# Optimization experiments

Hardware: AMD Instinct MI355X
Metric: run time of the kernel (lower is better)

The kernel has to match this reference:

```python
import jax, jax.numpy as jnp
import numpy as np

B, C, H, W = 4, 256, 32, 32
NUM_HEADS = 8
DK = C // NUM_HEADS


def _conv1x1(x_bcn, Wt, b):
    # x_bcn: [B, C, N]; Wt: [C_out, C_in]; b: [C_out]
    return jnp.einsum('oc,bcn->bon', Wt, x_bcn) + b[None, :, None]


def setup_inputs() -> dict:
    key = jax.random.key(0)
    ks = jax.random.split(key, 12)
    shp = (B, C, H, W)
    s = 1.0 / np.sqrt(C)
    return {
        'x0': jax.random.normal(ks[0], shp, jnp.float32),
        'x1': jax.random.normal(ks[1], shp, jnp.float32),
        'x2': jax.random.normal(ks[2], shp, jnp.float32),
        'gamma': jnp.ones((1,), jnp.float32),
        'gamma_1': jnp.ones((1,), jnp.float32),
        'gamma_2': jnp.ones((1,), jnp.float32),
        'Wq': jax.random.normal(ks[3], (C, C), jnp.float32) * s,
        'bq': jnp.zeros((C,), jnp.float32),
        'Wk': jax.random.normal(ks[4], (C, C), jnp.float32) * s,
        'bk': jnp.zeros((C,), jnp.float32),
        'Wv': jax.random.normal(ks[5], (C, C), jnp.float32) * s,
        'bv': jnp.zeros((C,), jnp.float32),
        'Wo': jax.random.normal(ks[6], (C, C), jnp.float32) * s,
        'bo': jnp.zeros((C,), jnp.float32),
    }


def reference(x0, x1, x2, gamma, gamma_1, gamma_2, Wq, bq, Wk, bk, Wv, bv, Wo, bo):
    h, dk = NUM_HEADS, DK
    N = H * W
    s0 = gamma * x0
    s1 = gamma_1 * x1
    s2 = gamma_2 * x2
    s0f = s0.reshape(B, C, N)
    streams = jnp.stack([s0f, s1.reshape(B, C, N), s2.reshape(B, C, N)], axis=1)  # [B,3,C,N]
    # Q: [B, h, N, dk]
    Q = _conv1x1(s0f, Wq, bq).reshape(B, h, dk, N).transpose(0, 1, 3, 2)
    kv_in = streams.reshape(B * 3, C, N)
    # K, V: [B, 3, h, dk, N] -> [B, h, 3N, dk]
    K = _conv1x1(kv_in, Wk, bk).reshape(B, 3, h, dk, N).transpose(0, 2, 1, 4, 3).reshape(B, h, 3 * N, dk)
    V = _conv1x1(kv_in, Wv, bv).reshape(B, 3, h, dk, N).transpose(0, 2, 1, 4, 3).reshape(B, h, 3 * N, dk)
    scores = jnp.einsum('bhqd,bhkd->bhqk', Q, K) / jnp.sqrt(jnp.float32(dk))  # [B,h,N,3N]
    attn = jax.nn.softmax(scores, axis=-1)
    out = jnp.einsum('bhqk,bhkd->bhqd', attn, V)  # [B,h,N,dk]
    out = out.transpose(0, 1, 3, 2).reshape(B, C, N)  # [B,C,N]
    fused = _conv1x1(out, Wo, bo).reshape(B, C, H, W)
    return fused
```

## Files before the change

kernel.cpp:

```cpp
#include <hip/hip_runtime.h>

typedef short bf16x8 __attribute__((ext_vector_type(8)));
typedef float f32x4  __attribute__((ext_vector_type(4)));
typedef short sh4    __attribute__((ext_vector_type(4)));
typedef float fl4    __attribute__((ext_vector_type(4)));
typedef unsigned u32x2 __attribute__((ext_vector_type(2)));
typedef unsigned u32x4 __attribute__((ext_vector_type(4)));

#define B_N  4
#define C_N  256
#define NH_N 8
#define DK_N 32
#define N_N  1024
#define KN_N 3072

#if defined(__has_builtin)
#if __has_builtin(__builtin_amdgcn_permlane32_swap) && __has_builtin(__builtin_amdgcn_permlane16_swap)
#define USE_PERMLANE 1
#endif
#endif
#ifndef USE_PERMLANE
#define USE_PERMLANE 0
#endif

__device__ __forceinline__ short f2bf(float f) {
    union { float f; unsigned u; } v; v.f = f;
    unsigned r = v.u + 0x7fffu + ((v.u >> 16) & 1u);
    return (short)(r >> 16);
}
__device__ __forceinline__ unsigned fbits(float f) {
    union { float f; unsigned u; } v; v.f = f; return v.u;
}

__device__ __forceinline__ int stg_idx(int c, int n) {
    return c * 64 + ((((n >> 2) ^ (c >> 2)) & 15) << 2) + (n & 3);
}

__global__ __launch_bounds__(256) void prep_kernel(
    const float* __restrict__ x0, const float* __restrict__ x1,
    const float* __restrict__ x2, const float* __restrict__ g0,
    const float* __restrict__ g1, const float* __restrict__ g2,
    const float* __restrict__ Wq, const float* __restrict__ Wk,
    const float* __restrict__ Wv, const float* __restrict__ Wo,
    short* __restrict__ Xt, short* __restrict__ Wbf) {
    __shared__ float stage[4096];
    int bx = blockIdx.x, t = threadIdx.x;
    if (bx >= 192) {
        int e = (bx - 192) * 4096 + t * 16;
        int m = e >> 16, off = e & 65535;
        const float* src = (m == 0) ? Wq : (m == 1) ? Wk : (m == 2) ? Wv : Wo;
        short* dst = Wbf + m * 65536 + off;
#pragma unroll
        for (int j = 0; j < 4; ++j) {
            fl4 v = *reinterpret_cast<const fl4*>(src + off + j * 4);
            sh4 o;
            o.x = f2bf(v.x); o.y = f2bf(v.y); o.z = f2bf(v.z); o.w = f2bf(v.w);
            *reinterpret_cast<sh4*>(dst + j * 4) = o;
        }
        return;
    }
    int bs = bx >> 4;
    int n0 = (bx & 15) << 6;
    int b = bs / 3, s = bs - b * 3;
    const float* xs = (s == 0) ? x0 : (s == 1) ? x1 : x2;
    float g = (s == 0) ? g0[0] : (s == 1) ? g1[0] : g2[0];
    const float* srcb = xs + (size_t)b * C_N * N_N;
    int n4 = (t & 15) << 2;
    for (int ch = 0; ch < 4; ++ch) {
        int c0 = ch << 6;
#pragma unroll
        for (int r = 0; r < 4; ++r) {
            int cl = (t >> 4) + (r << 4);
            fl4 v = *reinterpret_cast<const fl4*>(srcb + (size_t)(c0 + cl) * N_N + n0 + n4);
            v.x *= g; v.y *= g; v.z *= g; v.w *= g;
            *reinterpret_cast<fl4*>(&stage[stg_idx(cl, n4)]) = v;
        }
        __syncthreads();
#pragma unroll
        for (int j = 0; j < 2; ++j) {
            int u = t + (j << 8);
            int nl = u >> 3, cg = (u & 7) << 3;
            union { bf16x8 v8; short s16[8]; } pk;
#pragma unroll
            for (int i = 0; i < 8; ++i) pk.s16[i] = f2bf(stage[stg_idx(cg + i, nl)]);
            size_t rowsh = ((size_t)bs * N_N + n0 + nl) * C_N;
            unsigned cb = ((unsigned)((c0 + cg) * 2)) ^ ((unsigned)((nl & 7) << 4));
            *reinterpret_cast<bf16x8*>((char*)Xt + rowsh * 2 + cb) = pk.v8;
        }
        __syncthreads();
    }
}

__global__ __launch_bounds__(256) void qkv_kernel(
    const short* __restrict__ Wbf, const float* __restrict__ bq,
    const float* __restrict__ bk, const float* __restrict__ bv,
    const short* __restrict__ Xt,
    short* __restrict__ Qs, short* __restrict__ Ks, short* __restrict__ Vt) {
    __shared__ short Bt[16384];
    int b = blockIdx.z, mt = blockIdx.y, ct = blockIdx.x;
    int s = ct >> 4, n0 = (ct & 15) << 6;
    int t = threadIdx.x, lane = t & 63, w = t >> 6;
    int l16 = lane & 15, quad = lane >> 4;
    int m0 = mt << 6;
    bool hasQ = (s == 0);

    const char* gsrc = (const char*)(Xt + (((size_t)(b * 3 + s)) * N_N + n0) * C_N);
    char* ldst = (char*)Bt;
#pragma unroll
    for (int i = 0; i < 8; ++i) {
        int off = ((w << 3) + i) << 10;
        __builtin_amdgcn_global_load_lds(
            (const __attribute__((address_space(1))) void*)(gsrc + off + lane * 16),
            (__attribute__((address_space(3))) void*)(ldst + off), 16, 0, 0);
    }
    __syncthreads();

    f32x4 aq[4], ak[4], av[4];
#pragma unroll
    for (int i = 0; i < 4; ++i) {
        aq[i] = f32x4{0.f, 0.f, 0.f, 0.f};
        ak[i] = f32x4{0.f, 0.f, 0.f, 0.f};
        av[i] = f32x4{0.f, 0.f, 0.f, 0.f};
    }
    const short* WqA = Wbf;
    const short* WkA = Wbf + 65536;
    const short* WvA = Wbf + 131072;
    int arow = m0 + (w << 4) + l16;
    unsigned xv = (unsigned)((l16 & 7) << 4);
    const char* btb = (const char*)Bt;
#pragma unroll
    for (int kc = 0; kc < 256; kc += 32) {
        unsigned colb = ((unsigned)((kc + quad * 8) * 2)) ^ xv;
        bf16x8 bt0 = *reinterpret_cast<const bf16x8*>(btb + ((0  + l16) << 9) + colb);
        bf16x8 bt1 = *reinterpret_cast<const bf16x8*>(btb + ((16 + l16) << 9) + colb);
        bf16x8 bt2 = *reinterpret_cast<const bf16x8*>(btb + ((32 + l16) << 9) + colb);
        bf16x8 bt3 = *reinterpret_cast<const bf16x8*>(btb + ((48 + l16) << 9) + colb);
        bf16x8 wk = *reinterpret_cast<const bf16x8*>(WkA + (size_t)arow * C_N + kc + quad * 8);
        ak[0] = __builtin_amdgcn_mfma_f32_16x16x32_bf16(wk, bt0, ak[0], 0, 0, 0);
        ak[1] = __builtin_amdgcn_mfma_f32_16x16x32_bf16(wk, bt1, ak[1], 0, 0, 0);
        ak[2] = __builtin_amdgcn_mfma_f32_16x16x32_bf16(wk, bt2, ak[2], 0, 0, 0);
        ak[3] = __builtin_amdgcn_mfma_f32_16x16x32_bf16(wk, bt3, ak[3], 0, 0, 0);
        bf16x8 wv = *reinterpret_cast<const bf16x8*>(WvA + (size_t)arow * C_N + kc + quad * 8);
        av[0] = __builtin_amdgcn_mfma_f32_16x16x32_bf16(wv, bt0, av[0], 0, 0, 0);
        av[1] = __builtin_amdgcn_mfma_f32_16x16x32_bf16(wv, bt1, av[1], 0, 0, 0);
        av[2] = __builtin_amdgcn_mfma_f32_16x16x32_bf16(wv, bt2, av[2], 0, 0, 0);
        av[3] = __builtin_amdgcn_mfma_f32_16x16x32_bf16(wv, bt3, av[3], 0, 0, 0);
        if (hasQ) {
            bf16x8 wq = *reinterpret_cast<const bf16x8*>(WqA + (size_t)arow * C_N + kc + quad * 8);
            aq[0] = __builtin_amdgcn_mfma_f32_16x16x32_bf16(wq, bt0, aq[0], 0, 0, 0);
            aq[1] = __builtin_amdgcn_mfma_f32_16x16x32_bf16(wq, bt1, aq[1], 0, 0, 0);
            aq[2] = __builtin_amdgcn_mfma_f32_16x16x32_bf16(wq, bt2, aq[2], 0, 0, 0);
            aq[3] = __builtin_amdgcn_mfma_f32_16x16x32_bf16(wq, bt3, aq[3], 0, 0, 0);
        }
    }
    __syncthreads();

    short* SMq = Bt;
    short* SMk = Bt + 5120;
    short* SMv = Bt + 10240;
    int row0 = m0 + (w << 4) + (quad << 2);
    int dk0 = ((w & 1) << 4) + (quad << 2);
    {
        float kb0 = bk[row0], kb1 = bk[row0 + 1], kb2 = bk[row0 + 2], kb3 = bk[row0 + 3];
        short* Tp = SMk + (w >> 1) * 2560 + dk0;
#pragma unroll
        for (int nt = 0; nt < 4; ++nt) {
            int pos = (nt << 4) + l16;
            sh4 pk;
            pk.x = f2bf(ak[nt][0] + kb0); pk.y = f2bf(ak[nt][1] + kb1);
            pk.z = f2bf(ak[nt][2] + kb2); pk.w = f2bf(ak[nt][3] + kb3);
            *reinterpret_cast<sh4*>(Tp + pos * 40) = pk;
        }
    }
    if (hasQ) {
        const float QSCALE = 0.17677669529663687f * 1.4426950408889634f;
        float qb0 = bq[row0], qb1 = bq[row0 + 1], qb2 = bq[row0 + 2], qb3 = bq[row0 + 3];
        short* Tp = SMq + (w >> 1) * 2560 + dk0;
#pragma unroll
        for (int nt = 0; nt < 4; ++nt) {
            int pos = (nt << 4) + l16;
            sh4 pk;
            pk.x = f2bf((aq[nt][0] + qb0) * QSCALE); pk.y = f2bf((aq[nt][1] + qb1) * QSCALE);
            pk.z = f2bf((aq[nt][2] + qb2) * QSCALE); pk.w = f2bf((aq[nt][3] + qb3) * QSCALE);
            *reinterpret_cast<sh4*>(Tp + pos * 40) = pk;
        }
    }
    {
        int crow = (w << 4) + (quad << 2);
        float vb0 = bv[m0 + crow], vb1 = bv[m0 + crow + 1];
        float vb2 = bv[m0 + crow + 2], vb3 = bv[m0 + crow + 3];
#pragma unroll
        for (int nt = 0; nt < 4; ++nt) {
            int pos = (nt << 4) + l16;
            SMv[(crow + 0) * 72 + pos] = f2bf(av[nt][0] + vb0);
            SMv[(crow + 1) * 72 + pos] = f2bf(av[nt][1] + vb1);
            SMv[(crow + 2) * 72 + pos] = f2bf(av[nt][2] + vb2);
            SMv[(crow + 3) * 72 + pos] = f2bf(av[nt][3] + vb3);
        }
    }
    __syncthreads();

    {
        int pos_l = t >> 2, seg = t & 3;
#pragma unroll
        for (int hl = 0; hl < 2; ++hl) {
            int h = 2 * mt + hl;
            bf16x8 kv = *reinterpret_cast<const bf16x8*>(SMk + hl * 2560 + pos_l * 40 + seg * 8);
            *reinterpret_cast<bf16x8*>(
                Ks + ((size_t)(b * NH_N + h) * KN_N + s * N_N + n0) * DK_N + t * 8) = kv;
            if (hasQ) {
                bf16x8 qv = *reinterpret_cast<const bf16x8*>(SMq + hl * 2560 + pos_l * 40 + seg * 8);
                *reinterpret_cast<bf16x8*>(
                    Qs + ((size_t)(b * NH_N + h) * N_N + n0) * DK_N + t * 8) = qv;
            }
        }
#pragma unroll
        for (int i = 0; i < 2; ++i) {
            int chn = t + (i << 8);
            int row = chn >> 3, seg2 = chn & 7;
            bf16x8 vv = *reinterpret_cast<const bf16x8*>(SMv + row * 72 + seg2 * 8);
            int co = m0 + row;
            int h = co >> 5, d = co & 31;
            *reinterpret_cast<bf16x8*>(
                Vt + ((size_t)(b * NH_N + h) * DK_N + d) * KN_N + s * N_N + n0 + seg2 * 8) = vv;
        }
    }
}

struct Frags { bf16x8 k0, k1, k2, k3, v00, v01, v10, v11; };

__device__ __forceinline__ Frags ldfr(const short* Kp, const short* Vp0, int k0) {
    Frags f;
    f.k0  = *reinterpret_cast<const bf16x8*>(Kp + (k0 +  0) * DK_N);
    f.k1  = *reinterpret_cast<const bf16x8*>(Kp + (k0 + 16) * DK_N);
    f.k2  = *reinterpret_cast<const bf16x8*>(Kp + (k0 + 32) * DK_N);
    f.k3  = *reinterpret_cast<const bf16x8*>(Kp + (k0 + 48) * DK_N);
    f.v00 = *reinterpret_cast<const bf16x8*>(Vp0 + k0);
    f.v01 = *reinterpret_cast<const bf16x8*>(Vp0 + 16 * KN_N + k0);
    f.v10 = *reinterpret_cast<const bf16x8*>(Vp0 + k0 + 32);
    f.v11 = *reinterpret_cast<const bf16x8*>(Vp0 + 16 * KN_N + k0 + 32);
    return f;
}

#define EXPPACK(sv, Ra, Rb, LACC) {                             \
    float p0 = __builtin_amdgcn_exp2f(sv[0]);                   \
    float p1 = __builtin_amdgcn_exp2f(sv[1]);                   \
    float p2 = __builtin_amdgcn_exp2f(sv[2]);                   \
    float p3 = __builtin_amdgcn_exp2f(sv[3]);                   \
    LACC += (p0 + p1) + (p2 + p3);                              \
    Ra = __builtin_amdgcn_perm(fbits(p1), fbits(p0), 0x07060302u); \
    Rb = __builtin_amdgcn_perm(fbits(p3), fbits(p2), 0x07060302u); \
}

#if USE_PERMLANE
#define PVSTEP(RA0, RA1, RB0, RB1, VF0, VF1, O0, O1) {                 \
    unsigned x0 = RA0, y0 = RB0, x1 = RA1, y1 = RB1;                   \
    u32x2 r_;                                                          \
    r_ = __builtin_amdgcn_permlane32_swap(x0, y0, false, false); x0 = r_.x; y0 = r_.y; \
    r_ = __builtin_amdgcn_permlane16_swap(x0, y0, false, false); x0 = r_.x; y0 = r_.y; \
    r_ = __builtin_amdgcn_permlane32_swap(x1, y1, false, false); x1 = r_.x; y1 = r_.y; \
    r_ = __builtin_amdgcn_permlane16_swap(x1, y1, false, false); x1 = r_.x; y1 = r_.y; \
    union { u32x4 u; bf16x8 b; } pf_; pf_.u = u32x4{x0, x1, y0, y1};   \
    __builtin_amdgcn_s_setprio(1);                                     \
    O0 = __builtin_amdgcn_mfma_f32_16x16x32_bf16(VF0, pf_.b, O0, 0, 0, 0); \
    O1 = __builtin_amdgcn_mfma_f32_16x16x32_bf16(VF1, pf_.b, O1, 0, 0, 0); \
    __builtin_amdgcn_s_setprio(0);                                     \
}
#else
#define PVSTEP(RA0, RA1, RB0, RB1, VF0, VF1, O0, O1) {                 \
    union { u32x2 u; sh4 s; } wa_, wb_;                                \
    wa_.u = u32x2{RA0, RA1}; wb_.u = u32x2{RB0, RB1};                  \
    *reinterpret_cast<sh4*>(&PT[w][l16][quad * 4])      = wa_.s;       \
    *reinterpret_cast<sh4*>(&PT[w][l16][16 + quad * 4]) = wb_.s;       \
    bf16x8 pf_ = *reinterpret_cast<bf16x8*>(&PT[w][l16][quad * 8]);    \
    O0 = __builtin_amdgcn_mfma_f32_16x16x32_bf16(VF0, pf_, O0, 0, 0, 0); \
    O1 = __builtin_amdgcn_mfma_f32_16x16x32_bf16(VF1, pf_, O1, 0, 0, 0); \
}
#endif

#define PROCJ(f, QF, LACC, O0, O1) {                                     \
    __builtin_amdgcn_s_setprio(1);                                       \
    f32x4 s0 = __builtin_amdgcn_mfma_f32_16x16x32_bf16(f.k0, QF, zero, 0, 0, 0); \
    f32x4 s1 = __builtin_amdgcn_mfma_f32_16x16x32_bf16(f.k1, QF, zero, 0, 0, 0); \
    f32x4 s2 = __builtin_amdgcn_mfma_f32_16x16x32_bf16(f.k2, QF, zero, 0, 0, 0); \
    f32x4 s3 = __builtin_amdgcn_mfma_f32_16x16x32_bf16(f.k3, QF, zero, 0, 0, 0); \
    __builtin_amdgcn_s_setprio(0);                                       \
    unsigned R00, R01, R10, R11, R20, R21, R30, R31;                     \
    EXPPACK(s0, R00, R01, LACC); EXPPACK(s1, R10, R11, LACC);            \
    EXPPACK(s2, R20, R21, LACC); EXPPACK(s3, R30, R31, LACC);            \
    PVSTEP(R00, R01, R10, R11, f.v00, f.v01, O0, O1);                    \
    PVSTEP(R20, R21, R30, R31, f.v10, f.v11, O0, O1);                    \
}

#define PROCALL(f) {                                                     \
    PROCJ(f, qf0, la0, o00, o01);                                        \
    PROCJ(f, qf1, la1, o10, o11);                                        \
    PROCJ(f, qf2, la2, o20, o21);                                        \
    PROCJ(f, qf3, la3, o30, o31);                                        \
}

__global__ __launch_bounds__(256, 2) void attn_kernel(
    const short* __restrict__ Qs, const short* __restrict__ Ks,
    const short* __restrict__ Vt, short* __restrict__ Ot) {
    __shared__ float OL[4][64][36];
    __shared__ float Ll[4][64];
#if !USE_PERMLANE
    __shared__ short PT[4][16][36];
#endif

    int bh = blockIdx.x;
    int q0 = blockIdx.y * 64;
    int t = threadIdx.x, lane = t & 63, w = t >> 6;
    int l16 = lane & 15, quad = lane >> 4;

    const short* Qbase = Qs + ((size_t)bh * N_N + q0 + l16) * DK_N + quad * 8;
    bf16x8 qf0 = *reinterpret_cast<const bf16x8*>(Qbase + 0 * 16 * DK_N);
    bf16x8 qf1 = *reinterpret_cast<const bf16x8*>(Qbase + 1 * 16 * DK_N);
    bf16x8 qf2 = *reinterpret_cast<const bf16x8*>(Qbase + 2 * 16 * DK_N);
    bf16x8 qf3 = *reinterpret_cast<const bf16x8*>(Qbase + 3 * 16 * DK_N);
    const short* Kp  = Ks + ((size_t)bh * KN_N + l16) * DK_N + quad * 8;
    const short* Vp0 = Vt + ((size_t)bh * DK_N + l16) * KN_N + quad * 8;

    const f32x4 zero = {0.f, 0.f, 0.f, 0.f};
    f32x4 o00 = zero, o01 = zero, o10 = zero, o11 = zero;
    f32x4 o20 = zero, o21 = zero, o30 = zero, o31 = zero;
    float la0 = 0.f, la1 = 0.f, la2 = 0.f, la3 = 0.f;
    int kbase = w * 768;

    Frags cur = ldfr(Kp, Vp0, kbase);
#pragma unroll 2
    for (int i = 0; i < 11; ++i) {
        Frags nxt = ldfr(Kp, Vp0, kbase + (i + 1) * 64);
        PROCALL(cur);
        cur = nxt;
    }
    PROCALL(cur);

    la0 += __shfl_xor(la0, 16); la0 += __shfl_xor(la0, 32);
    la1 += __shfl_xor(la1, 16); la1 += __shfl_xor(la1, 32);
    la2 += __shfl_xor(la2, 16); la2 += __shfl_xor(la2, 32);
    la3 += __shfl_xor(la3, 16); la3 += __shfl_xor(la3, 32);

    *reinterpret_cast<fl4*>(&OL[w][ 0 + l16][quad * 4])      = o00;
    *reinterpret_cast<fl4*>(&OL[w][ 0 + l16][16 + quad * 4]) = o01;
    *reinterpret_cast<fl4*>(&OL[w][16 + l16][quad * 4])      = o10;
    *reinterpret_cast<fl4*>(&OL[w][16 + l16][16 + quad * 4]) = o11;
    *reinterpret_cast<fl4*>(&OL[w][32 + l16][quad * 4])      = o20;
    *reinterpret_cast<fl4*>(&OL[w][32 + l16][16 + quad * 4]) = o21;
    *reinterpret_cast<fl4*>(&OL[w][48 + l16][quad * 4])      = o30;
    *reinterpret_cast<fl4*>(&OL[w][48 + l16][16 + quad * 4]) = o31;
    if (quad == 0) {
        Ll[w][ 0 + l16] = la0;
        Ll[w][16 + l16] = la1;
        Ll[w][32 + l16] = la2;
        Ll[w][48 + l16] = la3;
    }
    __syncthreads();

    int q = t >> 2, d0 = (t & 3) * 8;
    float rl = 1.0f / (Ll[0][q] + Ll[1][q] + Ll[2][q] + Ll[3][q]);
    fl4 a0 = *reinterpret_cast<fl4*>(&OL[0][q][d0]);
    fl4 a1 = *reinterpret_cast<fl4*>(&OL[0][q][d0 + 4]);
#pragma unroll
    for (int s = 1; s < 4; ++s) {
        fl4 b0 = *reinterpret_cast<fl4*>(&OL[s][q][d0]);
        fl4 b1 = *reinterpret_cast<fl4*>(&OL[s][q][d0 + 4]);
        a0.x += b0.x; a0.y += b0.y; a0.z += b0.z; a0.w += b0.w;
        a1.x += b1.x; a1.y += b1.y; a1.z += b1.z; a1.w += b1.w;
    }
    union { sh4 s[2]; bf16x8 v; } pk;
    pk.s[0].x = f2bf(a0.x * rl); pk.s[0].y = f2bf(a0.y * rl);
    pk.s[0].z = f2bf(a0.z * rl); pk.s[0].w = f2bf(a0.w * rl);
    pk.s[1].x = f2bf(a1.x * rl); pk.s[1].y = f2bf(a1.y * rl);
    pk.s[1].z = f2bf(a1.z * rl); pk.s[1].w = f2bf(a1.w * rl);
    int b = bh >> 3, h = bh & 7;
    *reinterpret_cast<bf16x8*>(
        Ot + ((size_t)b * N_N + q0 + q) * C_N + h * DK_N + d0) = pk.v;
}

__global__ __launch_bounds__(256) void oproj_kernel(
    const short* __restrict__ Wo_bf, const float* __restrict__ bo,
    const short* __restrict__ Ot, float* __restrict__ out) {
    __shared__ float OS[64][36];
    int b = blockIdx.z, mt = blockIdx.y, ct = blockIdx.x;
    int t = threadIdx.x;
    int lane = t & 63, w = t >> 6;
    int l16 = lane & 15, quad = lane >> 4;
    int m0 = mt * 64, n0 = ct * 32;
    const short* Bsrc = Ot + ((size_t)b * N_N + n0) * C_N;
    int arow = m0 + w * 16 + l16;

    f32x4 acc[2];
    acc[0] = f32x4{0.f, 0.f, 0.f, 0.f};
    acc[1] = f32x4{0.f, 0.f, 0.f, 0.f};

#pragma unroll
    for (int kc = 0; kc < 256; kc += 32) {
        bf16x8 a = *reinterpret_cast<const bf16x8*>(Wo_bf + arow * C_N + kc + quad * 8);
#pragma unroll
        for (int nt = 0; nt < 2; ++nt) {
            bf16x8 bb = *reinterpret_cast<const bf16x8*>(Bsrc + (nt * 16 + l16) * C_N + kc + quad * 8);
            acc[nt] = __builtin_amdgcn_mfma_f32_16x16x32_bf16(a, bb, acc[nt], 0, 0, 0);
        }
    }

#pragma unroll
    for (int r = 0; r < 4; ++r) {
        int row_l = w * 16 + quad * 4 + r;
        float bias = bo[m0 + row_l];
        OS[row_l][l16]      = acc[0][r] + bias;
        OS[row_l][16 + l16] = acc[1][r] + bias;
    }
    __syncthreads();

    int row_l = t >> 2, seg = t & 3;
    fl4 v0 = *reinterpret_cast<fl4*>(&OS[row_l][seg * 8]);
    fl4 v1 = *reinterpret_cast<fl4*>(&OS[row_l][seg * 8 + 4]);
    float* dst = out + ((size_t)b * C_N + m0 + row_l) * N_N + n0 + seg * 8;
    *reinterpret_cast<fl4*>(dst)     = v0;
    *reinterpret_cast<fl4*>(dst + 4) = v1;
}

extern "C" void kernel_launch(void* const* d_in, const int* in_sizes, int n_in,
                              void* d_out, int out_size, void* d_ws, size_t ws_size,
                              hipStream_t stream) {
    const float* x0 = (const float*)d_in[0];
    const float* x1 = (const float*)d_in[1];
    const float* x2 = (const float*)d_in[2];
    const float* g0 = (const float*)d_in[3];
    const float* g1 = (const float*)d_in[4];
    const float* g2 = (const float*)d_in[5];
    const float* Wq = (const float*)d_in[6];
    const float* bq = (const float*)d_in[7];
    const float* Wk = (const float*)d_in[8];
    const float* bk = (const float*)d_in[9];
    const float* Wv = (const float*)d_in[10];
    const float* bv = (const float*)d_in[11];
    const float* Wo = (const float*)d_in[12];
    const float* bo = (const float*)d_in[13];
    float* out = (float*)d_out;

    char* wsb = (char*)d_ws;
    short* Wbf = (short*)(wsb + 0);
    short* Xt  = (short*)(wsb + 524288);
    short* Qs  = (short*)(wsb + 6815744);
    short* Ks  = (short*)(wsb + 8912896);
    short* Vt  = (short*)(wsb + 15204352);
    short* Ot  = (short*)(wsb + 21495808);

    prep_kernel<<<256, 256, 0, stream>>>(x0, x1, x2, g0, g1, g2,
                                         Wq, Wk, Wv, Wo, Xt, Wbf);
    qkv_kernel<<<dim3(48, 4, 4), 256, 0, stream>>>(Wbf, bq, bk, bv, Xt,
                                                   Qs, Ks, Vt);
    attn_kernel<<<dim3(32, 16), 256, 0, stream>>>(Qs, Ks, Vt, Ot);
    oproj_kernel<<<dim3(32, 4, 4), 256, 0, stream>>>(Wbf + 3 * 65536, bo, Ot, out);
}
```

Before: 133.1 us.

## Fuse all four stages into one cooperative kernel with grid-wide syncs

Merges the prep, QKV projection, attention and output projection kernels into a single cooperative launch of 512 blocks that separates the stages with grid.sync(). The aim is to remove the launch gaps and tail drains between four separate kernel launches. The QKV stage now loops over work units, because 768 tiles no longer map one-to-one onto blocks. If the cooperative launch fails, the code falls back to the original four launches. In exchange, every stage runs at a fixed grid size under the tighter occupancy limit, and the grid barriers add their own cost.

```diff
diff --git a/kernel.cpp b/kernel.cpp
--- a/kernel.cpp
+++ b/kernel.cpp
@@ -1,4 +1,7 @@
 #include <hip/hip_runtime.h>
+#include <hip/hip_cooperative_groups.h>
+
+namespace cg = cooperative_groups;
 
 typedef short bf16x8 __attribute__((ext_vector_type(8)));
 typedef float f32x4  __attribute__((ext_vector_type(4)));
@@ -34,6 +37,399 @@
 
 __device__ __forceinline__ int stg_idx(int c, int n) {
     return c * 64 + ((((n >> 2) ^ (c >> 2)) & 15) << 2) + (n & 3);
+}
+
+struct Frags { bf16x8 k0, k1, k2, k3, v00, v01, v10, v11; };
+
+__device__ __forceinline__ Frags ldfr(const short* Kp, const short* Vp0, int k0) {
+    Frags f;
+    f.k0  = *reinterpret_cast<const bf16x8*>(Kp + (k0 +  0) * DK_N);
+    f.k1  = *reinterpret_cast<const bf16x8*>(Kp + (k0 + 16) * DK_N);
+    f.k2  = *reinterpret_cast<const bf16x8*>(Kp + (k0 + 32) * DK_N);
+    f.k3  = *reinterpret_cast<const bf16x8*>(Kp + (k0 + 48) * DK_N);
+    f.v00 = *reinterpret_cast<const bf16x8*>(Vp0 + k0);
+    f.v01 = *reinterpret_cast<const bf16x8*>(Vp0 + 16 * KN_N + k0);
+    f.v10 = *reinterpret_cast<const bf16x8*>(Vp0 + k0 + 32);
+    f.v11 = *reinterpret_cast<const bf16x8*>(Vp0 + 16 * KN_N + k0 + 32);
+    return f;
+}
+
+#define EXPPACK(sv, Ra, Rb, LACC) {                             \
+    float p0 = __builtin_amdgcn_exp2f(sv[0]);                   \
+    float p1 = __builtin_amdgcn_exp2f(sv[1]);                   \
+    float p2 = __builtin_amdgcn_exp2f(sv[2]);                   \
+    float p3 = __builtin_amdgcn_exp2f(sv[3]);                   \
+    LACC += (p0 + p1) + (p2 + p3);                              \
+    Ra = __builtin_amdgcn_perm(fbits(p1), fbits(p0), 0x07060302u); \
+    Rb = __builtin_amdgcn_perm(fbits(p3), fbits(p2), 0x07060302u); \
+}
+
+#if USE_PERMLANE
+#define PVSTEP(RA0, RA1, RB0, RB1, VF0, VF1, O0, O1) {                 \
+    unsigned x0 = RA0, y0 = RB0, x1 = RA1, y1 = RB1;                   \
+    u32x2 r_;                                                          \
+    r_ = __builtin_amdgcn_permlane32_swap(x0, y0, false, false); x0 = r_.x; y0 = r_.y; \
+    r_ = __builtin_amdgcn_permlane16_swap(x0, y0, false, false); x0 = r_.x; y0 = r_.y; \
+    r_ = __builtin_amdgcn_permlane32_swap(x1, y1, false, false); x1 = r_.x; y1 = r_.y; \
+    r_ = __builtin_amdgcn_permlane16_swap(x1, y1, false, false); x1 = r_.x; y1 = r_.y; \
+    union { u32x4 u; bf16x8 b; } pf_; pf_.u = u32x4{x0, x1, y0, y1};   \
+    __builtin_amdgcn_s_setprio(1);                                     \
+    O0 = __builtin_amdgcn_mfma_f32_16x16x32_bf16(VF0, pf_.b, O0, 0, 0, 0); \
+    O1 = __builtin_amdgcn_mfma_f32_16x16x32_bf16(VF1, pf_.b, O1, 0, 0, 0); \
+    __builtin_amdgcn_s_setprio(0);                                     \
+}
+#else
+#define PVSTEP(RA0, RA1, RB0, RB1, VF0, VF1, O0, O1) {                 \
+    union { u32x2 u; sh4 s; } wa_, wb_;                                \
+    wa_.u = u32x2{RA0, RA1}; wb_.u = u32x2{RB0, RB1};                  \
+    *reinterpret_cast<sh4*>(&PT[w][l16][quad * 4])      = wa_.s;       \
+    *reinterpret_cast<sh4*>(&PT[w][l16][16 + quad * 4]) = wb_.s;       \
+    bf16x8 pf_ = *reinterpret_cast<bf16x8*>(&PT[w][l16][quad * 8]);    \
+    O0 = __builtin_amdgcn_mfma_f32_16x16x32_bf16(VF0, pf_, O0, 0, 0, 0); \
+    O1 = __builtin_amdgcn_mfma_f32_16x16x32_bf16(VF1, pf_, O1, 0, 0, 0); \
+}
+#endif
+
+#define PROCJ(f, QF, LACC, O0, O1) {                                     \
+    __builtin_amdgcn_s_setprio(1);                                       \
+    f32x4 s0 = __builtin_amdgcn_mfma_f32_16x16x32_bf16(f.k0, QF, zero, 0, 0, 0); \
+    f32x4 s1 = __builtin_amdgcn_mfma_f32_16x16x32_bf16(f.k1, QF, zero, 0, 0, 0); \
+    f32x4 s2 = __builtin_amdgcn_mfma_f32_16x16x32_bf16(f.k2, QF, zero, 0, 0, 0); \
+    f32x4 s3 = __builtin_amdgcn_mfma_f32_16x16x32_bf16(f.k3, QF, zero, 0, 0, 0); \
+    __builtin_amdgcn_s_setprio(0);                                       \
+    unsigned R00, R01, R10, R11, R20, R21, R30, R31;                     \
+    EXPPACK(s0, R00, R01, LACC); EXPPACK(s1, R10, R11, LACC);            \
+    EXPPACK(s2, R20, R21, LACC); EXPPACK(s3, R30, R31, LACC);            \
+    PVSTEP(R00, R01, R10, R11, f.v00, f.v01, O0, O1);                    \
+    PVSTEP(R20, R21, R30, R31, f.v10, f.v11, O0, O1);                    \
+}
+
+#define PROCALL(f) {                                                     \
+    PROCJ(f, qf0, la0, o00, o01);                                        \
+    PROCJ(f, qf1, la1, o10, o11);                                        \
+    PROCJ(f, qf2, la2, o20, o21);                                        \
+    PROCJ(f, qf3, la3, o30, o31);                                        \
+}
+
+__global__ __launch_bounds__(256, 2) void fused_all(
+    const float* __restrict__ x0, const float* __restrict__ x1,
+    const float* __restrict__ x2, const float* __restrict__ g0,
+    const float* __restrict__ g1, const float* __restrict__ g2,
+    const float* __restrict__ Wq, const float* __restrict__ Wk,
+    const float* __restrict__ Wv, const float* __restrict__ Wo,
+    const float* __restrict__ bq, const float* __restrict__ bk,
+    const float* __restrict__ bv, const float* __restrict__ bo,
+    short* __restrict__ Wbf, short* __restrict__ Xt,
+    short* __restrict__ Qs, short* __restrict__ Ks,
+    short* __restrict__ Vt, short* __restrict__ Ot,
+    float* __restrict__ out) {
+    __shared__ __align__(16) char smem[42496];
+    cg::grid_group grid = cg::this_grid();
+    int bid = blockIdx.x;
+    int t = threadIdx.x;
+
+    {
+        float* stage = reinterpret_cast<float*>(smem);
+        if (bid >= 192 && bid < 256) {
+            int e = (bid - 192) * 4096 + t * 16;
+            int m = e >> 16, off = e & 65535;
+            const float* src = (m == 0) ? Wq : (m == 1) ? Wk : (m == 2) ? Wv : Wo;
+            short* dst = Wbf + m * 65536 + off;
+#pragma unroll
+            for (int j = 0; j < 4; ++j) {
+                fl4 v = *reinterpret_cast<const fl4*>(src + off + j * 4);
+                sh4 o;
+                o.x = f2bf(v.x); o.y = f2bf(v.y); o.z = f2bf(v.z); o.w = f2bf(v.w);
+                *reinterpret_cast<sh4*>(dst + j * 4) = o;
+            }
+        } else if (bid < 192) {
+            int bs = bid >> 4;
+            int n0 = (bid & 15) << 6;
+            int b = bs / 3, s = bs - b * 3;
+            const float* xs = (s == 0) ? x0 : (s == 1) ? x1 : x2;
+            float g = (s == 0) ? g0[0] : (s == 1) ? g1[0] : g2[0];
+            const float* srcb = xs + (size_t)b * C_N * N_N;
+            int n4 = (t & 15) << 2;
+            for (int ch = 0; ch < 4; ++ch) {
+                int c0 = ch << 6;
+#pragma unroll
+                for (int r = 0; r < 4; ++r) {
+                    int cl = (t >> 4) + (r << 4);
+                    fl4 v = *reinterpret_cast<const fl4*>(srcb + (size_t)(c0 + cl) * N_N + n0 + n4);
+                    v.x *= g; v.y *= g; v.z *= g; v.w *= g;
+                    *reinterpret_cast<fl4*>(&stage[stg_idx(cl, n4)]) = v;
+                }
+                __syncthreads();
+#pragma unroll
+                for (int j = 0; j < 2; ++j) {
+                    int u = t + (j << 8);
+                    int nl = u >> 3, cg2 = (u & 7) << 3;
+                    union { bf16x8 v8; short s16[8]; } pk;
+#pragma unroll
+                    for (int i = 0; i < 8; ++i) pk.s16[i] = f2bf(stage[stg_idx(cg2 + i, nl)]);
+                    size_t rowsh = ((size_t)bs * N_N + n0 + nl) * C_N;
+                    unsigned cb = ((unsigned)((c0 + cg2) * 2)) ^ ((unsigned)((nl & 7) << 4));
+                    *reinterpret_cast<bf16x8*>((char*)Xt + rowsh * 2 + cb) = pk.v8;
+                }
+                __syncthreads();
+            }
+        }
+    }
+    grid.sync();
+
+    {
+        short* Bt = reinterpret_cast<short*>(smem);
+        int lane = t & 63, w = t >> 6;
+        int l16 = lane & 15, quad = lane >> 4;
+        for (int u = bid; u < 768; u += 512) {
+            int ct = u % 48, mt = (u / 48) & 3, b = u / 192;
+            int s = ct >> 4, n0 = (ct & 15) << 6;
+            int m0 = mt << 6;
+            bool hasQ = (s == 0);
+            __syncthreads();
+
+            const char* gsrc = (const char*)(Xt + (((size_t)(b * 3 + s)) * N_N + n0) * C_N);
+            char* ldst = (char*)Bt;
+#pragma unroll
+            for (int i = 0; i < 8; ++i) {
+                int off = ((w << 3) + i) << 10;
+                __builtin_amdgcn_global_load_lds(
+                    (const __attribute__((address_space(1))) void*)(gsrc + off + lane * 16),
+                    (__attribute__((address_space(3))) void*)(ldst + off), 16, 0, 0);
+            }
+            __syncthreads();
+
+            f32x4 aq[4], ak[4], av[4];
+#pragma unroll
+            for (int i = 0; i < 4; ++i) {
+                aq[i] = f32x4{0.f, 0.f, 0.f, 0.f};
+                ak[i] = f32x4{0.f, 0.f, 0.f, 0.f};
+                av[i] = f32x4{0.f, 0.f, 0.f, 0.f};
+            }
+            const short* WqA = Wbf;
+            const short* WkA = Wbf + 65536;
+            const short* WvA = Wbf + 131072;
+            int arow = m0 + (w << 4) + l16;
+            unsigned xv = (unsigned)((l16 & 7) << 4);
+            const char* btb = (const char*)Bt;
+#pragma unroll
+            for (int kc = 0; kc < 256; kc += 32) {
+                unsigned colb = ((unsigned)((kc + quad * 8) * 2)) ^ xv;
+                bf16x8 bt0 = *reinterpret_cast<const bf16x8*>(btb + ((0  + l16) << 9) + colb);
+                bf16x8 bt1 = *reinterpret_cast<const bf16x8*>(btb + ((16 + l16) << 9) + colb);
+                bf16x8 bt2 = *reinterpret_cast<const bf16x8*>(btb + ((32 + l16) << 9) + colb);
+                bf16x8 bt3 = *reinterpret_cast<const bf16x8*>(btb + ((48 + l16) << 9) + colb);
+                bf16x8 wk = *reinterpret_cast<const bf16x8*>(WkA + (size_t)arow * C_N + kc + quad * 8);
+                ak[0] = __builtin_amdgcn_mfma_f32_16x16x32_bf16(wk, bt0, ak[0], 0, 0, 0);
+                ak[1] = __builtin_amdgcn_mfma_f32_16x16x32_bf16(wk, bt1, ak[1], 0, 0, 0);
+                ak[2] = __builtin_amdgcn_mfma_f32_16x16x32_bf16(wk, bt2, ak[2], 0, 0, 0);
+                ak[3] = __builtin_amdgcn_mfma_f32_16x16x32_bf16(wk, bt3, ak[3], 0, 0, 0);
+                bf16x8 wv = *reinterpret_cast<const bf16x8*>(WvA + (size_t)arow * C_N + kc + quad * 8);
+                av[0] = __builtin_amdgcn_mfma_f32_16x16x32_bf16(wv, bt0, av[0], 0, 0, 0);
+                av[1] = __builtin_amdgcn_mfma_f32_16x16x32_bf16(wv, bt1, av[1], 0, 0, 0);
+                av[2] = __builtin_amdgcn_mfma_f32_16x16x32_bf16(wv, bt2, av[2], 0, 0, 0);
+                av[3] = __builtin_amdgcn_mfma_f32_16x16x32_bf16(wv, bt3, av[3], 0, 0, 0);
+                if (hasQ) {
+                    bf16x8 wq = *reinterpret_cast<const bf16x8*>(WqA + (size_t)arow * C_N + kc + quad * 8);
+                    aq[0] = __builtin_amdgcn_mfma_f32_16x16x32_bf16(wq, bt0, aq[0], 0, 0, 0);
+                    aq[1] = __builtin_amdgcn_mfma_f32_16x16x32_bf16(wq, bt1, aq[1], 0, 0, 0);
+                    aq[2] = __builtin_amdgcn_mfma_f32_16x16x32_bf16(wq, bt2, aq[2], 0, 0, 0);
+                    aq[3] = __builtin_amdgcn_mfma_f32_16x16x32_bf16(wq, bt3, aq[3], 0, 0, 0);
+                }
+            }
+            __syncthreads();
+
+            short* SMq = Bt;
+            short* SMk = Bt + 5120;
+            short* SMv = Bt + 10240;
+            int row0 = m0 + (w << 4) + (quad << 2);
+            int dk0 = ((w & 1) << 4) + (quad << 2);
+            {
+                float kb0 = bk[row0], kb1 = bk[row0 + 1], kb2 = bk[row0 + 2], kb3 = bk[row0 + 3];
+                short* Tp = SMk + (w >> 1) * 2560 + dk0;
+#pragma unroll
+                for (int nt = 0; nt < 4; ++nt) {
+                    int pos = (nt << 4) + l16;
+                    sh4 pk;
+                    pk.x = f2bf(ak[nt][0] + kb0); pk.y = f2bf(ak[nt][1] + kb1);
+                    pk.z = f2bf(ak[nt][2] + kb2); pk.w = f2bf(ak[nt][3] + kb3);
+                    *reinterpret_cast<sh4*>(Tp + pos * 40) = pk;
+                }
+            }
+            if (hasQ) {
+                const float QSCALE = 0.17677669529663687f * 1.4426950408889634f;
+                float qb0 = bq[row0], qb1 = bq[row0 + 1], qb2 = bq[row0 + 2], qb3 = bq[row0 + 3];
+                short* Tp = SMq + (w >> 1) * 2560 + dk0;
+#pragma unroll
+                for (int nt = 0; nt < 4; ++nt) {
+                    int pos = (nt << 4) + l16;
+                    sh4 pk;
+                    pk.x = f2bf((aq[nt][0] + qb0) * QSCALE); pk.y = f2bf((aq[nt][1] + qb1) * QSCALE);
+                    pk.z = f2bf((aq[nt][2] + qb2) * QSCALE); pk.w = f2bf((aq[nt][3] + qb3) * QSCALE);
+                    *reinterpret_cast<sh4*>(Tp + pos * 40) = pk;
+                }
+            }
+            {
+                int crow = (w << 4) + (quad << 2);
+                float vb0 = bv[m0 + crow], vb1 = bv[m0 + crow + 1];
+                float vb2 = bv[m0 + crow + 2], vb3 = bv[m0 + crow + 3];
+#pragma unroll
+                for (int nt = 0; nt < 4; ++nt) {
+                    int pos = (nt << 4) + l16;
+                    SMv[(crow + 0) * 72 + pos] = f2bf(av[nt][0] + vb0);
+                    SMv[(crow + 1) * 72 + pos] = f2bf(av[nt][1] + vb1);
+                    SMv[(crow + 2) * 72 + pos] = f2bf(av[nt][2] + vb2);
+                    SMv[(crow + 3) * 72 + pos] = f2bf(av[nt][3] + vb3);
+                }
+            }
+            __syncthreads();
+            {
+                int pos_l = t >> 2, seg = t & 3;
+#pragma unroll
+                for (int hl = 0; hl < 2; ++hl) {
+                    int h = 2 * mt + hl;
+                    bf16x8 kv = *reinterpret_cast<const bf16x8*>(SMk + hl * 2560 + pos_l * 40 + seg * 8);
+                    *reinterpret_cast<bf16x8*>(
+                        Ks + ((size_t)(b * NH_N + h) * KN_N + s * N_N + n0) * DK_N + t * 8) = kv;
+                    if (hasQ) {
+                        bf16x8 qv = *reinterpret_cast<const bf16x8*>(SMq + hl * 2560 + pos_l * 40 + seg * 8);
+                        *reinterpret_cast<bf16x8*>(
+                            Qs + ((size_t)(b * NH_N + h) * N_N + n0) * DK_N + t * 8) = qv;
+                    }
+                }
+#pragma unroll
+                for (int i = 0; i < 2; ++i) {
+                    int chn = t + (i << 8);
+                    int row = chn >> 3, seg2 = chn & 7;
+                    bf16x8 vv = *reinterpret_cast<const bf16x8*>(SMv + row * 72 + seg2 * 8);
+                    int co = m0 + row;
+                    int h = co >> 5, d = co & 31;
+                    *reinterpret_cast<bf16x8*>(
+                        Vt + ((size_t)(b * NH_N + h) * DK_N + d) * KN_N + s * N_N + n0 + seg2 * 8) = vv;
+                }
+            }
+        }
+    }
+    grid.sync();
+
+    {
+        typedef float OLarr[64][36];
+        OLarr* OL = reinterpret_cast<OLarr*>(smem);
+        float (*Ll)[64] = reinterpret_cast<float(*)[64]>(smem + 36864);
+#if !USE_PERMLANE
+        typedef short PTarr[16][36];
+        PTarr* PT = reinterpret_cast<PTarr*>(smem + 37888);
+#endif
+        int bh = bid >> 4;
+        int q0 = (bid & 15) * 64;
+        int lane = t & 63, w = t >> 6;
+        int l16 = lane & 15, quad = lane >> 4;
+
+        const short* Qbase = Qs + ((size_t)bh * N_N + q0 + l16) * DK_N + quad * 8;
+        bf16x8 qf0 = *reinterpret_cast<const bf16x8*>(Qbase + 0 * 16 * DK_N);
+        bf16x8 qf1 = *reinterpret_cast<const bf16x8*>(Qbase + 1 * 16 * DK_N);
+        bf16x8 qf2 = *reinterpret_cast<const bf16x8*>(Qbase + 2 * 16 * DK_N);
+        bf16x8 qf3 = *reinterpret_cast<const bf16x8*>(Qbase + 3 * 16 * DK_N);
+        const short* Kp  = Ks + ((size_t)bh * KN_N + l16) * DK_N + quad * 8;
+        const short* Vp0 = Vt + ((size_t)bh * DK_N + l16) * KN_N + quad * 8;
+
+        const f32x4 zero = {0.f, 0.f, 0.f, 0.f};
+        f32x4 o00 = zero, o01 = zero, o10 = zero, o11 = zero;
+        f32x4 o20 = zero, o21 = zero, o30 = zero, o31 = zero;
+        float la0 = 0.f, la1 = 0.f, la2 = 0.f, la3 = 0.f;
+        int kbase = w * 768;
+
+        Frags cur = ldfr(Kp, Vp0, kbase);
+#pragma unroll 2
+        for (int i = 0; i < 11; ++i) {
+            Frags nxt = ldfr(Kp, Vp0, kbase + (i + 1) * 64);
+            PROCALL(cur);
+            cur = nxt;
+        }
+        PROCALL(cur);
+
+        la0 += __shfl_xor(la0, 16); la0 += __shfl_xor(la0, 32);
+        la1 += __shfl_xor(la1, 16); la1 += __shfl_xor(la1, 32);
+        la2 += __shfl_xor(la2, 16); la2 += __shfl_xor(la2, 32);
+        la3 += __shfl_xor(la3, 16); la3 += __shfl_xor(la3, 32);
+
+        __syncthreads();
+        *reinterpret_cast<fl4*>(&OL[w][ 0 + l16][quad * 4])      = o00;
+        *reinterpret_cast<fl4*>(&OL[w][ 0 + l16][16 + quad * 4]) = o01;
+        *reinterpret_cast<fl4*>(&OL[w][16 + l16][quad * 4])      = o10;
+        *reinterpret_cast<fl4*>(&OL[w][16 + l16][16 + quad * 4]) = o11;
+        *reinterpret_cast<fl4*>(&OL[w][32 + l16][quad * 4])      = o20;
+        *reinterpret_cast<fl4*>(&OL[w][32 + l16][16 + quad * 4]) = o21;
+        *reinterpret_cast<fl4*>(&OL[w][48 + l16][quad * 4])      = o30;
+        *reinterpret_cast<fl4*>(&OL[w][48 + l16][16 + quad * 4]) = o31;
+        if (quad == 0) {
+            Ll[w][ 0 + l16] = la0;
+            Ll[w][16 + l16] = la1;
+            Ll[w][32 + l16] = la2;
+            Ll[w][48 + l16] = la3;
+        }
+        __syncthreads();
+
+        int q = t >> 2, d0 = (t & 3) * 8;
+        float rl = 1.0f / (Ll[0][q] + Ll[1][q] + Ll[2][q] + Ll[3][q]);
+        fl4 a0 = *reinterpret_cast<fl4*>(&OL[0][q][d0]);
+        fl4 a1 = *reinterpret_cast<fl4*>(&OL[0][q][d0 + 4]);
+#pragma unroll
+        for (int sp = 1; sp < 4; ++sp) {
+            fl4 b0 = *reinterpret_cast<fl4*>(&OL[sp][q][d0]);
+            fl4 b1 = *reinterpret_cast<fl4*>(&OL[sp][q][d0 + 4]);
+            a0.x += b0.x; a0.y += b0.y; a0.z += b0.z; a0.w += b0.w;
+            a1.x += b1.x; a1.y += b1.y; a1.z += b1.z; a1.w += b1.w;
+        }
+        union { sh4 s[2]; bf16x8 v; } pk;
+        pk.s[0].x = f2bf(a0.x * rl); pk.s[0].y = f2bf(a0.y * rl);
+        pk.s[0].z = f2bf(a0.z * rl); pk.s[0].w = f2bf(a0.w * rl);
+        pk.s[1].x = f2bf(a1.x * rl); pk.s[1].y = f2bf(a1.y * rl);
+        pk.s[1].z = f2bf(a1.z * rl); pk.s[1].w = f2bf(a1.w * rl);
+        int b = bh >> 3, h = bh & 7;
+        *reinterpret_cast<bf16x8*>(
+            Ot + ((size_t)b * N_N + q0 + q) * C_N + h * DK_N + d0) = pk.v;
+    }
+    grid.sync();
+
+    {
+        float (*OS)[36] = reinterpret_cast<float(*)[36]>(smem);
+        int ct = bid & 31, mt = (bid >> 5) & 3, b = bid >> 7;
+        int lane = t & 63, w = t >> 6;
+        int l16 = lane & 15, quad = lane >> 4;
+        int m0 = mt * 64, n0 = ct * 32;
+        const short* Bsrc = Ot + ((size_t)b * N_N + n0) * C_N;
+        int arow = m0 + w * 16 + l16;
+        const short* Wo_bf = Wbf + 3 * 65536;
+
+        f32x4 acc[2];
+        acc[0] = f32x4{0.f, 0.f, 0.f, 0.f};
+        acc[1] = f32x4{0.f, 0.f, 0.f, 0.f};
+#pragma unroll
+        for (int kc = 0; kc < 256; kc += 32) {
+            bf16x8 a = *reinterpret_cast<const bf16x8*>(Wo_bf + arow * C_N + kc + quad * 8);
+#pragma unroll
+            for (int nt = 0; nt < 2; ++nt) {
+                bf16x8 bb = *reinterpret_cast<const bf16x8*>(Bsrc + (nt * 16 + l16) * C_N + kc + quad * 8);
+                acc[nt] = __builtin_amdgcn_mfma_f32_16x16x32_bf16(a, bb, acc[nt], 0, 0, 0);
+            }
+        }
+        __syncthreads();
+#pragma unroll
+        for (int r = 0; r < 4; ++r) {
+            int row_l = w * 16 + quad * 4 + r;
+            float bias = bo[m0 + row_l];
+            OS[row_l][l16]      = acc[0][r] + bias;
+            OS[row_l][16 + l16] = acc[1][r] + bias;
+        }
+        __syncthreads();
+        int row_l = t >> 2, seg = t & 3;
+        fl4 v0 = *reinterpret_cast<fl4*>(&OS[row_l][seg * 8]);
+        fl4 v1 = *reinterpret_cast<fl4*>(&OS[row_l][seg * 8 + 4]);
+        float* dst = out + ((size_t)b * C_N + m0 + row_l) * N_N + n0 + seg * 8;
+        *reinterpret_cast<fl4*>(dst)     = v0;
+        *reinterpret_cast<fl4*>(dst + 4) = v1;
+    }
 }
 
 __global__ __launch_bounds__(256) void prep_kernel(
@@ -79,12 +475,12 @@
 #pragma unroll
         for (int j = 0; j < 2; ++j) {
             int u = t + (j << 8);
-            int nl = u >> 3, cg = (u & 7) << 3;
+            int nl = u >> 3, cg2 = (u & 7) << 3;
             union { bf16x8 v8; short s16[8]; } pk;
 #pragma unroll
-            for (int i = 0; i < 8; ++i) pk.s16[i] = f2bf(stage[stg_idx(cg + i, nl)]);
+            for (int i = 0; i < 8; ++i) pk.s16[i] = f2bf(stage[stg_idx(cg2 + i, nl)]);
             size_t rowsh = ((size_t)bs * N_N + n0 + nl) * C_N;
-            unsigned cb = ((unsigned)((c0 + cg) * 2)) ^ ((unsigned)((nl & 7) << 4));
+            unsigned cb = ((unsigned)((c0 + cg2) * 2)) ^ ((unsigned)((nl & 7) << 4));
             *reinterpret_cast<bf16x8*>((char*)Xt + rowsh * 2 + cb) = pk.v8;
         }
         __syncthreads();
@@ -199,7 +595,6 @@
         }
     }
     __syncthreads();
-
     {
         int pos_l = t >> 2, seg = t & 3;
 #pragma unroll
@@ -227,78 +622,6 @@
     }
 }
 
-struct Frags { bf16x8 k0, k1, k2, k3, v00, v01, v10, v11; };
-
-__device__ __forceinline__ Frags ldfr(const short* Kp, const short* Vp0, int k0) {
-    Frags f;
-    f.k0  = *reinterpret_cast<const bf16x8*>(Kp + (k0 +  0) * DK_N);
-    f.k1  = *reinterpret_cast<const bf16x8*>(Kp + (k0 + 16) * DK_N);
-    f.k2  = *reinterpret_cast<const bf16x8*>(Kp + (k0 + 32) * DK_N);
-    f.k3  = *reinterpret_cast<const bf16x8*>(Kp + (k0 + 48) * DK_N);
-    f.v00 = *reinterpret_cast<const bf16x8*>(Vp0 + k0);
-    f.v01 = *reinterpret_cast<const bf16x8*>(Vp0 + 16 * KN_N + k0);
-    f.v10 = *reinterpret_cast<const bf16x8*>(Vp0 + k0 + 32);
-    f.v11 = *reinterpret_cast<const bf16x8*>(Vp0 + 16 * KN_N + k0 + 32);
-    return f;
-}
-
-#define EXPPACK(sv, Ra, Rb, LACC) {                             \
-    float p0 = __builtin_amdgcn_exp2f(sv[0]);                   \
-    float p1 = __builtin_amdgcn_exp2f(sv[1]);                   \
-    float p2 = __builtin_amdgcn_exp2f(sv[2]);                   \
-    float p3 = __builtin_amdgcn_exp2f(sv[3]);                   \
-    LACC += (p0 + p1) + (p2 + p3);                              \
-    Ra = __builtin_amdgcn_perm(fbits(p1), fbits(p0), 0x07060302u); \
-    Rb = __builtin_amdgcn_perm(fbits(p3), fbits(p2), 0x07060302u); \
-}
-
-#if USE_PERMLANE
-#define PVSTEP(RA0, RA1, RB0, RB1, VF0, VF1, O0, O1) {                 \
-    unsigned x0 = RA0, y0 = RB0, x1 = RA1, y1 = RB1;                   \
-    u32x2 r_;                                                          \
-    r_ = __builtin_amdgcn_permlane32_swap(x0, y0, false, false); x0 = r_.x; y0 = r_.y; \
-    r_ = __builtin_amdgcn_permlane16_swap(x0, y0, false, false); x0 = r_.x; y0 = r_.y; \
-    r_ = __builtin_amdgcn_permlane32_swap(x1, y1, false, false); x1 = r_.x; y1 = r_.y; \
-    r_ = __builtin_amdgcn_permlane16_swap(x1, y1, false, false); x1 = r_.x; y1 = r_.y; \
-    union { u32x4 u; bf16x8 b; } pf_; pf_.u = u32x4{x0, x1, y0, y1};   \
-    __builtin_amdgcn_s_setprio(1);                                     \
-    O0 = __builtin_amdgcn_mfma_f32_16x16x32_bf16(VF0, pf_.b, O0, 0, 0, 0); \
-    O1 = __builtin_amdgcn_mfma_f32_16x16x32_bf16(VF1, pf_.b, O1, 0, 0, 0); \
-    __builtin_amdgcn_s_setprio(0);                                     \
-}
-#else
-#define PVSTEP(RA0, RA1, RB0, RB1, VF0, VF1, O0, O1) {                 \
-    union { u32x2 u; sh4 s; } wa_, wb_;                                \
-    wa_.u = u32x2{RA0, RA1}; wb_.u = u32x2{RB0, RB1};                  \
-    *reinterpret_cast<sh4*>(&PT[w][l16][quad * 4])      = wa_.s;       \
-    *reinterpret_cast<sh4*>(&PT[w][l16][16 + quad * 4]) = wb_.s;       \
-    bf16x8 pf_ = *reinterpret_cast<bf16x8*>(&PT[w][l16][quad * 8]);    \
-    O0 = __builtin_amdgcn_mfma_f32_16x16x32_bf16(VF0, pf_, O0, 0, 0, 0); \
-    O1 = __builtin_amdgcn_mfma_f32_16x16x32_bf16(VF1, pf_, O1, 0, 0, 0); \
-}
-#endif
-
-#define PROCJ(f, QF, LACC, O0, O1) {                                     \
-    __builtin_amdgcn_s_setprio(1);                                       \
-    f32x4 s0 = __builtin_amdgcn_mfma_f32_16x16x32_bf16(f.k0, QF, zero, 0, 0, 0); \
-    f32x4 s1 = __builtin_amdgcn_mfma_f32_16x16x32_bf16(f.k1, QF, zero, 0, 0, 0); \
-    f32x4 s2 = __builtin_amdgcn_mfma_f32_16x16x32_bf16(f.k2, QF, zero, 0, 0, 0); \
-    f32x4 s3 = __builtin_amdgcn_mfma_f32_16x16x32_bf16(f.k3, QF, zero, 0, 0, 0); \
-    __builtin_amdgcn_s_setprio(0);                                       \
-    unsigned R00, R01, R10, R11, R20, R21, R30, R31;                     \
-    EXPPACK(s0, R00, R01, LACC); EXPPACK(s1, R10, R11, LACC);            \
-    EXPPACK(s2, R20, R21, LACC); EXPPACK(s3, R30, R31, LACC);            \
-    PVSTEP(R00, R01, R10, R11, f.v00, f.v01, O0, O1);                    \
-    PVSTEP(R20, R21, R30, R31, f.v10, f.v11, O0, O1);                    \
-}
-
-#define PROCALL(f) {                                                     \
-    PROCJ(f, qf0, la0, o00, o01);                                        \
-    PROCJ(f, qf1, la1, o10, o11);                                        \
-    PROCJ(f, qf2, la2, o20, o21);                                        \
-    PROCJ(f, qf3, la3, o30, o31);                                        \
-}
-
 __global__ __launch_bounds__(256, 2) void attn_kernel(
     const short* __restrict__ Qs, const short* __restrict__ Ks,
     const short* __restrict__ Vt, short* __restrict__ Ot) {
@@ -307,7 +630,6 @@
 #if !USE_PERMLANE
     __shared__ short PT[4][16][36];
 #endif
-
     int bh = blockIdx.x;
     int q0 = blockIdx.y * 64;
     int t = threadIdx.x, lane = t & 63, w = t >> 6;
@@ -393,7 +715,6 @@
     f32x4 acc[2];
     acc[0] = f32x4{0.f, 0.f, 0.f, 0.f};
     acc[1] = f32x4{0.f, 0.f, 0.f, 0.f};
-
 #pragma unroll
     for (int kc = 0; kc < 256; kc += 32) {
         bf16x8 a = *reinterpret_cast<const bf16x8*>(Wo_bf + arow * C_N + kc + quad * 8);
@@ -403,7 +724,6 @@
             acc[nt] = __builtin_amdgcn_mfma_f32_16x16x32_bf16(a, bb, acc[nt], 0, 0, 0);
         }
     }
-
 #pragma unroll
     for (int r = 0; r < 4; ++r) {
         int row_l = w * 16 + quad * 4 + r;
@@ -412,7 +732,6 @@
         OS[row_l][16 + l16] = acc[1][r] + bias;
     }
     __syncthreads();
-
     int row_l = t >> 2, seg = t & 3;
     fl4 v0 = *reinterpret_cast<fl4*>(&OS[row_l][seg * 8]);
     fl4 v1 = *reinterpret_cast<fl4*>(&OS[row_l][seg * 8 + 4]);
@@ -448,10 +767,22 @@
     short* Vt  = (short*)(wsb + 15204352);
     short* Ot  = (short*)(wsb + 21495808);
 
-    prep_kernel<<<256, 256, 0, stream>>>(x0, x1, x2, g0, g1, g2,
-                                         Wq, Wk, Wv, Wo, Xt, Wbf);
-    qkv_kernel<<<dim3(48, 4, 4), 256, 0, stream>>>(Wbf, bq, bk, bv, Xt,
-                                                   Qs, Ks, Vt);
-    attn_kernel<<<dim3(32, 16), 256, 0, stream>>>(Qs, Ks, Vt, Ot);
-    oproj_kernel<<<dim3(32, 4, 4), 256, 0, stream>>>(Wbf + 3 * 65536, bo, Ot, out);
-}
+    void* args[] = {
+        (void*)&x0, (void*)&x1, (void*)&x2, (void*)&g0, (void*)&g1, (void*)&g2,
+        (void*)&Wq, (void*)&Wk, (void*)&Wv, (void*)&Wo,
+        (void*)&bq, (void*)&bk, (void*)&bv, (void*)&bo,
+        (void*)&Wbf, (void*)&Xt, (void*)&Qs, (void*)&Ks, (void*)&Vt, (void*)&Ot,
+        (void*)&out,
+    };
+    hipError_t e = hipLaunchCooperativeKernel(
+        (const void*)fused_all, dim3(512), dim3(256), args, 0, stream);
+    if (e != hipSuccess) {
+        (void)hipGetLastError();
+        prep_kernel<<<256, 256, 0, stream>>>(x0, x1, x2, g0, g1, g2,
+                                             Wq, Wk, Wv, Wo, Xt, Wbf);
+        qkv_kernel<<<dim3(48, 4, 4), 256, 0, stream>>>(Wbf, bq, bk, bv, Xt,
+                                                       Qs, Ks, Vt);
+        attn_kernel<<<dim3(32, 16), 256, 0, stream>>>(Qs, Ks, Vt, Ot);
+        oproj_kernel<<<dim3(32, 4, 4), 256, 0, stream>>>(Wbf + 3 * 65536, bo, Ot, out);
+    }
+}
```

Measured after the change: 313.4 us. +135.4%, slower.
